# Performance work log

Hardware: AMD Instinct MI355X
Metric: run time of the kernel (lower is better)

## Reference

```python
import jax, jax.numpy as jnp
import numpy as np

WINDOW_SIZE = 11
SIGMA = 1.5
C1 = 0.01 ** 2
C2 = 0.03 ** 2
MSE_WEIGHT = 1.0
SSIM_WEIGHT = 0.01


def _gaussian_window(channels):
    # 1D gaussian, normalized, then outer product -> [C,1,K,K] depthwise kernel
    coords = np.arange(WINDOW_SIZE) - WINDOW_SIZE // 2
    g = np.exp(-(coords ** 2) / (2.0 * SIGMA ** 2))
    g = g / g.sum()
    w2d = np.outer(g, g).astype(np.float32)  # [K,K]
    w = np.tile(w2d[None, None], (channels, 1, 1, 1))  # [C,1,K,K]
    return jnp.asarray(w)


def _depthwise_conv(x, w):
    # x: [B,C,H,W], w: [C,1,K,K]; SAME padding, groups=C (matches torch conv2d pad=K//2, groups=C)
    pad = WINDOW_SIZE // 2
    return jax.lax.conv_general_dilated(
        x, w,
        window_strides=(1, 1),
        padding=[(pad, pad), (pad, pad)],
        dimension_numbers=('NCHW', 'OIHW', 'NCHW'),
        feature_group_count=x.shape[1],
    )


def setup_inputs() -> dict:
    key = jax.random.key(0)
    k1, k2 = jax.random.split(key)
    shape = (32, 3, 512, 512)
    predicted = jax.random.uniform(k1, shape, dtype=jnp.float32)
    target = jax.random.uniform(k2, shape, dtype=jnp.float32)
    return {"predicted": predicted, "target": target}


def reference(predicted, target):
    # MSE part
    mse_l = jnp.mean((predicted - target) ** 2)

    # SSIM part (standard pytorch-ssim: gaussian window, size_average=True)
    C = predicted.shape[1]
    w = _gaussian_window(C)

    mu1 = _depthwise_conv(predicted, w)
    mu2 = _depthwise_conv(target, w)
    mu1_sq = mu1 * mu1
    mu2_sq = mu2 * mu2
    mu1_mu2 = mu1 * mu2

    sigma1_sq = _depthwise_conv(predicted * predicted, w) - mu1_sq
    sigma2_sq = _depthwise_conv(target * target, w) - mu2_sq
    sigma12 = _depthwise_conv(predicted * target, w) - mu1_mu2

    ssim_map = ((2.0 * mu1_mu2 + C1) * (2.0 * sigma12 + C2)) / (
        (mu1_sq + mu2_sq + C1) * (sigma1_sq + sigma2_sq + C2)
    )
    ssim_val = jnp.mean(ssim_map)

    return MSE_WEIGHT * mse_l + SSIM_WEIGHT * (1.0 - ssim_val)
```

## Files before the change

### kernel.cpp

```cpp
#include <hip/hip_runtime.h>
#include <hip/hip_fp16.h>


#define WSZ   512
#define TW    64
#define TH    16
#define HALO  5
#define IN_H  (TH + 2*HALO)
#define NPOS  32
#define GX    (WSZ / TW)
#define GY    (WSZ / TH)
#define NSLOT 64
#define SSIM_C1 0.0001f
#define SSIM_C2 0.0009f

#define W0 0.00102838f
#define W1 0.00759876f
#define W2 0.03600080f
#define W3 0.10936080f
#define W4 0.21300560f
#define W5 0.26601170f

static __device__ __forceinline__ __half2 pk(float a, float b) {
    return __builtin_bit_cast(__half2, __builtin_amdgcn_cvt_pkrtz(a, b));
}
static __device__ __forceinline__ __half2 stagger(__half2 hi, __half2 lo) {
    return __builtin_bit_cast(__half2,
        __builtin_amdgcn_alignbit(__builtin_bit_cast(unsigned, hi),
                                  __builtin_bit_cast(unsigned, lo), 16));
}

__launch_bounds__(256, 8)
__global__ void fused_mse_ssim(const float* __restrict__ P,
                               const float* __restrict__ T,
                               float* __restrict__ ws) {
    __shared__ float4 sAB[IN_H][NPOS];
    __shared__ float  red[2][4];

    const int tid = threadIdx.x;
    const int gx0 = blockIdx.x * TW;
    const int gy0 = blockIdx.y * TH;
    const size_t plane = (size_t)blockIdx.z * (WSZ * (size_t)WSZ);
    const float* Pp = P + plane;
    const float* Tp = T + plane;
    const bool xedge = (blockIdx.x == 0) || (blockIdx.x == GX - 1);

    const float gwf[11] = {W0,W1,W2,W3,W4,W5,W4,W3,W2,W1,W0};
    unsigned gwh[11];
    #pragma unroll
    for (int k = 0; k < 11; ++k)
        gwh[k] = __builtin_amdgcn_readfirstlane(
                     __builtin_bit_cast(unsigned, __float2half2_rn(gwf[k])));

    float mse = 0.f;

    if (tid < IN_H * 8) {
        const int r  = tid >> 3;
        const int q  = tid & 7;
        const int gy = gy0 - HALO + r;
        const int cb = gx0 + q * 8 - 8;
        const float* prow = Pp + ((long)gy * WSZ + cb);
        const float* trow = Tp + ((long)gy * WSZ + cb);
        const bool rv   = ((unsigned)gy < (unsigned)WSZ);
        const bool mrow = ((unsigned)(r - HALO) < (unsigned)TH);

        const __half2 z = __float2half2_rn(0.f);
        __half2 As[12], Ad[12];

        if (!xedge) {
            if (rv) {
                #pragma unroll
                for (int b = 0; b < 6; ++b) {
                    const float4 pv = *(const float4*)(prow + 4 * b);
                    const float4 tv = *(const float4*)(trow + 4 * b);
                    const float s0 = pv.x + tv.x, s1 = pv.y + tv.y;
                    const float s2 = pv.z + tv.z, s3 = pv.w + tv.w;
                    const float d0 = pv.x - tv.x, d1 = pv.y - tv.y;
                    const float d2 = pv.z - tv.z, d3 = pv.w - tv.w;
                    As[2*b]   = pk(s0, s1); As[2*b+1] = pk(s2, s3);
                    Ad[2*b]   = pk(d0, d1); Ad[2*b+1] = pk(d2, d3);
                    if ((b == 2 || b == 3) && mrow) {
                        mse = fmaf(d0, d0, mse); mse = fmaf(d1, d1, mse);
                        mse = fmaf(d2, d2, mse); mse = fmaf(d3, d3, mse);
                    }
                }
            } else {
                #pragma unroll
                for (int b = 0; b < 12; ++b) { As[b] = z; Ad[b] = z; }
            }
        } else {
            #pragma unroll
            for (int b = 0; b < 6; ++b) {
                const unsigned cc = (unsigned)(cb + 4 * b);
                float4 pv = make_float4(0.f, 0.f, 0.f, 0.f);
                float4 tv = make_float4(0.f, 0.f, 0.f, 0.f);
                if (rv && cc < (unsigned)WSZ) {
                    pv = *(const float4*)(prow + 4 * b);
                    tv = *(const float4*)(trow + 4 * b);
                }
                const float s0 = pv.x + tv.x, s1 = pv.y + tv.y;
                const float s2 = pv.z + tv.z, s3 = pv.w + tv.w;
                const float d0 = pv.x - tv.x, d1 = pv.y - tv.y;
                const float d2 = pv.z - tv.z, d3 = pv.w - tv.w;
                As[2*b]   = pk(s0, s1); As[2*b+1] = pk(s2, s3);
                Ad[2*b]   = pk(d0, d1); Ad[2*b+1] = pk(d2, d3);
                if ((b == 2 || b == 3) && mrow) {
                    mse = fmaf(d0, d0, mse); mse = fmaf(d1, d1, mse);
                    mse = fmaf(d2, d2, mse); mse = fmaf(d3, d3, mse);
                }
            }
        }

        __half2 aS[4]  = {z, z, z, z};
        __half2 aD[4]  = {z, z, z, z};
        __half2 aSS[4] = {z, z, z, z};
        __half2 aDD[4] = {z, z, z, z};

        #pragma unroll
        for (int jj = 0; jj <= 16; ++jj) {
            const int j = jj + 3;
            __half2 vs, vd;
            if (j & 1) {
                vs = stagger(As[(j >> 1) + 1], As[j >> 1]);
                vd = stagger(Ad[(j >> 1) + 1], Ad[j >> 1]);
            } else {
                vs = As[j >> 1];
                vd = Ad[j >> 1];
            }
            const __half2 vss = __hmul2(vs, vs);
            const __half2 vdd = __hmul2(vd, vd);
            #pragma unroll
            for (int m = 0; m < 4; ++m) {
                const int k = jj - 2 * m;
                if (k >= 0 && k < 11) {
                    const __half2 w = __builtin_bit_cast(__half2, gwh[k]);
                    aS[m]  = __hfma2(w, vs,  aS[m]);
                    aD[m]  = __hfma2(w, vd,  aD[m]);
                    aSS[m] = __hfma2(w, vss, aSS[m]);
                    aDD[m] = __hfma2(w, vdd, aDD[m]);
                }
            }
        }

        #pragma unroll
        for (int m = 0; m < 4; ++m)
            sAB[r][8 * m + q] = make_float4(
                __builtin_bit_cast(float, aS[m]),  __builtin_bit_cast(float, aD[m]),
                __builtin_bit_cast(float, aSS[m]), __builtin_bit_cast(float, aDD[m]));
    }
    __syncthreads();

    const int q2  = tid & 31;
    const int col = ((q2 & 3) << 3) | (q2 >> 2);
    const int y0  = (tid >> 5) << 1;

    const __half2 z2 = __float2half2_rn(0.f);
    __half2 acc[2][4];
    #pragma unroll
    for (int a = 0; a < 2; ++a) {
        acc[a][0] = z2; acc[a][1] = z2; acc[a][2] = z2; acc[a][3] = z2;
    }

    #pragma unroll
    for (int j = 0; j < 12; ++j) {
        const float4 ab = sAB[y0 + j][col];
        const __half2 hS  = __builtin_bit_cast(__half2, ab.x);
        const __half2 hD  = __builtin_bit_cast(__half2, ab.y);
        const __half2 hSS = __builtin_bit_cast(__half2, ab.z);
        const __half2 hDD = __builtin_bit_cast(__half2, ab.w);
        if (j < 11) {
            const __half2 w = __builtin_bit_cast(__half2, gwh[j]);
            acc[0][0] = __hfma2(w, hS,  acc[0][0]);
            acc[0][1] = __hfma2(w, hD,  acc[0][1]);
            acc[0][2] = __hfma2(w, hSS, acc[0][2]);
            acc[0][3] = __hfma2(w, hDD, acc[0][3]);
        }
        if (j >= 1) {
            const __half2 w = __builtin_bit_cast(__half2, gwh[j - 1]);
            acc[1][0] = __hfma2(w, hS,  acc[1][0]);
            acc[1][1] = __hfma2(w, hD,  acc[1][1]);
            acc[1][2] = __hfma2(w, hSS, acc[1][2]);
            acc[1][3] = __hfma2(w, hDD, acc[1][3]);
        }
    }

    float ssim = 0.f;
    #pragma unroll
    for (int a = 0; a < 2; ++a) {
        const float2 Av = __half22float2(acc[a][0]);
        const float2 Bv = __half22float2(acc[a][1]);
        const float2 Xv = __half22float2(acc[a][2]);
        const float2 Yv = __half22float2(acc[a][3]);
        #pragma unroll
        for (int e = 0; e < 2; ++e) {
            const float A = e ? Av.y : Av.x;
            const float B = e ? Bv.y : Bv.x;
            const float X = e ? Xv.y : Xv.x;
            const float Y = e ? Yv.y : Yv.x;
            const float a2 = A * A;
            const float b2 = B * B;
            const float P1 = a2 + b2;
            const float M1 = a2 - b2;
            const float num1 = fmaf(0.5f, M1, SSIM_C1);
            const float den1 = fmaf(0.5f, P1, SSIM_C1);
            const float num2 = fmaf(0.5f, (X - Y) - M1, SSIM_C2);
            const float den2 = fmaf(0.5f, (X + Y) - P1, SSIM_C2);
            ssim = fmaf(num1 * num2, __builtin_amdgcn_rcpf(den1 * den2), ssim);
        }
    }

    #pragma unroll
    for (int off = 32; off > 0; off >>= 1) {
        mse  += __shfl_down(mse, off);
        ssim += __shfl_down(ssim, off);
    }
    const int wid = tid >> 6;
    if ((tid & 63) == 0) { red[0][wid] = mse; red[1][wid] = ssim; }
    __syncthreads();
    if (tid == 0) {
        const float m = red[0][0] + red[0][1] + red[0][2] + red[0][3];
        const float s = red[1][0] + red[1][1] + red[1][2] + red[1][3];
        const int bid  = (blockIdx.z * gridDim.y + blockIdx.y) * gridDim.x + blockIdx.x;
        const int slot = (bid & (NSLOT - 1)) * 16;
        atomicAdd(&ws[slot + 0], m);
        atomicAdd(&ws[slot + 1], s);
    }
}

__global__ void finalize_loss(const float* __restrict__ ws,
                              float* __restrict__ out, float invN) {
    const int t = threadIdx.x;
    float m = ws[t * 16 + 0];
    float s = ws[t * 16 + 1];
    #pragma unroll
    for (int off = 32; off > 0; off >>= 1) {
        m += __shfl_down(m, off);
        s += __shfl_down(s, off);
    }
    if (t == 0) out[0] = m * invN + 0.01f * (1.f - s * invN);
}

extern "C" void kernel_launch(void* const* d_in, const int* in_sizes, int n_in,
                              void* d_out, int out_size, void* d_ws, size_t ws_size,
                              hipStream_t stream) {
    const float* P = (const float*)d_in[0];
    const float* T = (const float*)d_in[1];
    float* out = (float*)d_out;
    float* ws  = (float*)d_ws;

    const int planes = in_sizes[0] / (WSZ * WSZ);
    const float invN = 1.f / (float)in_sizes[0];

    (void)hipMemsetAsync(ws, 0, NSLOT * 16 * sizeof(float), stream);
    dim3 grid(GX, GY, planes);
    fused_mse_ssim<<<grid, 256, 0, stream>>>(P, T, ws);
    finalize_loss<<<1, 64, 0, stream>>>(ws, out, invN);
}
```

Before: 249.1 us.

## Compute vertical Gaussian pass with MFMA and taller tiles

```diff
diff --git a/kernel.cpp b/kernel.cpp
--- a/kernel.cpp
+++ b/kernel.cpp
@@ -4,10 +4,10 @@
 
 #define WSZ   512
 #define TW    64
-#define TH    16
+#define TH    32
 #define HALO  5
 #define IN_H  (TH + 2*HALO)
-#define NPOS  32
+#define BUFR  48
 #define GX    (WSZ / TW)
 #define GY    (WSZ / TH)
 #define NSLOT 64
@@ -21,8 +21,14 @@
 #define W4 0.21300560f
 #define W5 0.26601170f
 
+typedef _Float16 f16x4 __attribute__((ext_vector_type(4)));
+typedef float    f32x4 __attribute__((ext_vector_type(4)));
+
 static __device__ __forceinline__ __half2 pk(float a, float b) {
     return __builtin_bit_cast(__half2, __builtin_amdgcn_cvt_pkrtz(a, b));
+}
+static __device__ __forceinline__ unsigned pku(float a, float b) {
+    return __builtin_bit_cast(unsigned, __builtin_amdgcn_cvt_pkrtz(a, b));
 }
 static __device__ __forceinline__ __half2 stagger(__half2 hi, __half2 lo) {
     return __builtin_bit_cast(__half2,
@@ -30,11 +36,11 @@
                                   __builtin_bit_cast(unsigned, lo), 16));
 }
 
-__launch_bounds__(256, 8)
+__launch_bounds__(256, 6)
 __global__ void fused_mse_ssim(const float* __restrict__ P,
                                const float* __restrict__ T,
                                float* __restrict__ ws) {
-    __shared__ float4 sAB[IN_H][NPOS];
+    __shared__ float4 sAB[BUFR][32];
     __shared__ float  red[2][4];
 
     const int tid = threadIdx.x;
@@ -54,9 +60,12 @@
 
     float mse = 0.f;
 
-    if (tid < IN_H * 8) {
-        const int r  = tid >> 3;
-        const int q  = tid & 7;
+    if (tid < 192)
+        sAB[IN_H + (tid >> 5)][tid & 31] = make_float4(0.f, 0.f, 0.f, 0.f);
+
+    for (int it = tid; it < IN_H * 8; it += 256) {
+        const int r  = it >> 3;
+        const int q  = it & 7;
         const int gy = gy0 - HALO + r;
         const int cb = gx0 + q * 8 - 8;
         const float* prow = Pp + ((long)gy * WSZ + cb);
@@ -144,59 +153,98 @@
 
         #pragma unroll
         for (int m = 0; m < 4; ++m)
-            sAB[r][8 * m + q] = make_float4(
+            sAB[r][(4 * q + m + r) & 31] = make_float4(
                 __builtin_bit_cast(float, aS[m]),  __builtin_bit_cast(float, aD[m]),
                 __builtin_bit_cast(float, aSS[m]), __builtin_bit_cast(float, aDD[m]));
     }
     __syncthreads();
 
-    const int q2  = tid & 31;
-    const int col = ((q2 & 3) << 3) | (q2 >> 2);
-    const int y0  = (tid >> 5) << 1;
-
-    const __half2 z2 = __float2half2_rn(0.f);
-    __half2 acc[2][4];
-    #pragma unroll
-    for (int a = 0; a < 2; ++a) {
-        acc[a][0] = z2; acc[a][1] = z2; acc[a][2] = z2; acc[a][3] = z2;
-    }
-
-    #pragma unroll
-    for (int j = 0; j < 12; ++j) {
-        const float4 ab = sAB[y0 + j][col];
-        const __half2 hS  = __builtin_bit_cast(__half2, ab.x);
-        const __half2 hD  = __builtin_bit_cast(__half2, ab.y);
-        const __half2 hSS = __builtin_bit_cast(__half2, ab.z);
-        const __half2 hDD = __builtin_bit_cast(__half2, ab.w);
-        if (j < 11) {
-            const __half2 w = __builtin_bit_cast(__half2, gwh[j]);
-            acc[0][0] = __hfma2(w, hS,  acc[0][0]);
-            acc[0][1] = __hfma2(w, hD,  acc[0][1]);
-            acc[0][2] = __hfma2(w, hSS, acc[0][2]);
-            acc[0][3] = __hfma2(w, hDD, acc[0][3]);
-        }
-        if (j >= 1) {
-            const __half2 w = __builtin_bit_cast(__half2, gwh[j - 1]);
-            acc[1][0] = __hfma2(w, hS,  acc[1][0]);
-            acc[1][1] = __hfma2(w, hD,  acc[1][1]);
-            acc[1][2] = __hfma2(w, hSS, acc[1][2]);
-            acc[1][3] = __hfma2(w, hDD, acc[1][3]);
+    const int lane = tid & 63;
+    const int nT   = tid >> 6;
+    const int t    = lane >> 4;
+    const int colL = lane & 15;
+    const int x    = (nT << 4) | colL;
+    const int p    = x >> 1;
+    const unsigned sel = (x & 1) ? 0x07060302u : 0x05040100u;
+
+    f16x4 afrag[2];
+    #pragma unroll
+    for (int c = 0; c < 2; ++c) {
+        float av[4];
+        #pragma unroll
+        for (int i = 0; i < 4; ++i) {
+            const int idx = 16 * c + 4 * t + i - colL;
+            float v = 0.f;
+            #pragma unroll
+            for (int j = 0; j < 11; ++j) v = (idx == j) ? gwf[j] : v;
+            av[i] = v;
+        }
+        uint2 au;
+        au.x = pku(av[0], av[1]);
+        au.y = pku(av[2], av[3]);
+        afrag[c] = __builtin_bit_cast(f16x4, au);
+    }
+
+    f32x4 Dacc[2][4];
+    #pragma unroll
+    for (int m = 0; m < 2; ++m)
+        #pragma unroll
+        for (int f = 0; f < 4; ++f)
+            Dacc[m][f] = (f32x4){0.f, 0.f, 0.f, 0.f};
+
+    #pragma unroll
+    for (int bi = 0; bi < 3; ++bi) {
+        const int base = bi << 4;
+        float4 ld[4];
+        #pragma unroll
+        for (int i = 0; i < 4; ++i) {
+            const int r = base + 4 * t + i;
+            ld[i] = sAB[r][(p + r) & 31];
+        }
+        const unsigned* w0 = (const unsigned*)&ld[0];
+        const unsigned* w1 = (const unsigned*)&ld[1];
+        const unsigned* w2 = (const unsigned*)&ld[2];
+        const unsigned* w3 = (const unsigned*)&ld[3];
+
+        f16x4 bf[4];
+        #pragma unroll
+        for (int f = 0; f < 4; ++f) {
+            uint2 bu;
+            bu.x = __builtin_amdgcn_perm(w1[f], w0[f], sel);
+            bu.y = __builtin_amdgcn_perm(w3[f], w2[f], sel);
+            bf[f] = __builtin_bit_cast(f16x4, bu);
+        }
+
+        if (bi == 0) {
+            #pragma unroll
+            for (int f = 0; f < 4; ++f)
+                Dacc[0][f] = __builtin_amdgcn_mfma_f32_16x16x16f16(
+                                 afrag[0], bf[f], Dacc[0][f], 0, 0, 0);
+        } else if (bi == 1) {
+            #pragma unroll
+            for (int f = 0; f < 4; ++f) {
+                Dacc[0][f] = __builtin_amdgcn_mfma_f32_16x16x16f16(
+                                 afrag[1], bf[f], Dacc[0][f], 0, 0, 0);
+                Dacc[1][f] = __builtin_amdgcn_mfma_f32_16x16x16f16(
+                                 afrag[0], bf[f], Dacc[1][f], 0, 0, 0);
+            }
+        } else {
+            #pragma unroll
+            for (int f = 0; f < 4; ++f)
+                Dacc[1][f] = __builtin_amdgcn_mfma_f32_16x16x16f16(
+                                 afrag[1], bf[f], Dacc[1][f], 0, 0, 0);
         }
     }
 
     float ssim = 0.f;
     #pragma unroll
-    for (int a = 0; a < 2; ++a) {
-        const float2 Av = __half22float2(acc[a][0]);
-        const float2 Bv = __half22float2(acc[a][1]);
-        const float2 Xv = __half22float2(acc[a][2]);
-        const float2 Yv = __half22float2(acc[a][3]);
-        #pragma unroll
-        for (int e = 0; e < 2; ++e) {
-            const float A = e ? Av.y : Av.x;
-            const float B = e ? Bv.y : Bv.x;
-            const float X = e ? Xv.y : Xv.x;
-            const float Y = e ? Yv.y : Yv.x;
+    for (int m = 0; m < 2; ++m) {
+        #pragma unroll
+        for (int j = 0; j < 4; ++j) {
+            const float A = Dacc[m][0][j];
+            const float B = Dacc[m][1][j];
+            const float X = Dacc[m][2][j];
+            const float Y = Dacc[m][3][j];
             const float a2 = A * A;
             const float b2 = B * B;
             const float P1 = a2 + b2;
```

New measurement: 231.5 us. -7.1%, faster.
